# Kernel tuning notes

Measured on AMD Instinct MI355X. Metric: run time of the kernel, lower is better.

Reference implementation:

```python
import jax, jax.numpy as jnp
import numpy as np

N, F_IN, UNITS, HEADS = 8192, 256, 64, 4
NEG_BIG = -1e10


def setup_inputs() -> dict:
    key = jax.random.key(0)
    k1, k2, k3, k4, k5 = jax.random.split(key, 5)
    X = jax.random.normal(k1, (N, F_IN), dtype=jnp.float32)
    # sparse-ish binary adjacency with self-loops (float mask, as used by the module)
    A = (jax.random.uniform(k2, (N, N)) < 0.004).astype(jnp.float32)
    A = jnp.maximum(A, jnp.eye(N, dtype=jnp.float32))
    W = jax.random.normal(k3, (HEADS, F_IN, UNITS), dtype=jnp.float32) * (1.0 / np.sqrt(F_IN))
    attn_self = jax.random.normal(k4, (HEADS, UNITS), dtype=jnp.float32) * (1.0 / np.sqrt(UNITS))
    attn_neigh = jax.random.normal(k5, (HEADS, UNITS), dtype=jnp.float32) * (1.0 / np.sqrt(UNITS))
    return {"X": X, "A": A, "W": W, "attn_self": attn_self, "attn_neigh": attn_neigh}


def reference(X, A, W, attn_self, attn_neigh):
    # per-head linear projection: [H, N, U]
    feats = jnp.einsum('nf,hfu->hnu', X, W)
    a_self = jnp.einsum('hnu,hu->hn', feats, attn_self)    # [H, N]
    a_neigh = jnp.einsum('hnu,hu->hn', feats, attn_neigh)  # [H, N]
    # additive GAT scores: e_ij = a_self_i + a_neigh_j -> [H, N, N]
    scores = a_self[:, :, None] + a_neigh[:, None, :]
    scores = jax.nn.leaky_relu(scores, negative_slope=0.2)
    scores = scores + NEG_BIG * (1.0 - A)  # additive mask on non-edges
    attn = jax.nn.softmax(scores, axis=-1)
    # dropout is identity at training=False (module default)
    out = jnp.einsum('hnm,hmu->hnu', attn, feats)  # [H, N, U]
    # 'concat' reduction: head-major concat along feature dim -> [N, H*U]
    out = jnp.transpose(out, (1, 0, 2)).reshape(N, HEADS * UNITS)
    return jax.nn.elu(out)
```

## Files before the change

### kernel.cpp

```cpp
#include <hip/hip_runtime.h>
#include <hip/hip_bf16.h>

#define NN    8192
#define FIN   256
#define UNITS 64
#define HEADS 4
#define CTOT  256
#define CAP   256

__device__ __forceinline__ float bf2f(unsigned short u) {
    union { unsigned int i; float f; } v;
    v.i = ((unsigned int)u) << 16;
    return v.f;
}

__global__ void k_detect(const unsigned int* __restrict__ A, int* __restrict__ flag) {
    *flag = ((A[0] & 0xFFFFu) == 0x3F80u) ? 1 : 0;
}

__global__ __launch_bounds__(256) void k_proj(const void* __restrict__ Xv,
                                              const void* __restrict__ Wv,
                                              const int* __restrict__ flag,
                                              float* __restrict__ feats) {
    __shared__ float Xt[32 * 68];
    __shared__ float Wl[32 * 68];
    const int isbf = *flag;
    const int tid = threadIdx.x;
    const int r0  = blockIdx.x * 64;
    const int h   = blockIdx.y;

    const int r  = (tid & 15) * 4;
    const int cl = (tid >> 4) * 4;

    const int srow = tid >> 2;
    const int skq  = (tid & 3) * 8;
    const int wk   = tid >> 3;
    const int wu   = (tid & 7) * 8;

    float acc[4][4];
    #pragma unroll
    for (int a = 0; a < 4; ++a)
        #pragma unroll
        for (int b = 0; b < 4; ++b) acc[a][b] = 0.f;

    for (int k0 = 0; k0 < FIN; k0 += 32) {
        __syncthreads();
        if (isbf) {
            const unsigned short* X = (const unsigned short*)Xv;
            const unsigned short* W = (const unsigned short*)Wv;
            const uint4 xv = *reinterpret_cast<const uint4*>(
                X + (size_t)(r0 + srow) * FIN + k0 + skq);
            const unsigned int xs[4] = {xv.x, xv.y, xv.z, xv.w};
            #pragma unroll
            for (int m = 0; m < 4; ++m) {
                Xt[(skq + 2 * m    ) * 68 + srow] = bf2f((unsigned short)(xs[m] & 0xffffu));
                Xt[(skq + 2 * m + 1) * 68 + srow] = bf2f((unsigned short)(xs[m] >> 16));
            }
            const uint4 wv = *reinterpret_cast<const uint4*>(
                W + (size_t)h * (FIN * UNITS) + (size_t)(k0 + wk) * UNITS + wu);
            const unsigned int ws4[4] = {wv.x, wv.y, wv.z, wv.w};
            #pragma unroll
            for (int m = 0; m < 4; ++m) {
                Wl[wk * 68 + wu + 2 * m    ] = bf2f((unsigned short)(ws4[m] & 0xffffu));
                Wl[wk * 68 + wu + 2 * m + 1] = bf2f((unsigned short)(ws4[m] >> 16));
            }
        } else {
            const float* X = (const float*)Xv;
            const float* W = (const float*)Wv;
            const float4* xp = reinterpret_cast<const float4*>(
                X + (size_t)(r0 + srow) * FIN + k0 + skq);
            const float4 x0 = xp[0], x1 = xp[1];
            const float xs[8] = {x0.x, x0.y, x0.z, x0.w, x1.x, x1.y, x1.z, x1.w};
            #pragma unroll
            for (int m = 0; m < 8; ++m) Xt[(skq + m) * 68 + srow] = xs[m];
            const float4* wp = reinterpret_cast<const float4*>(
                W + (size_t)h * (FIN * UNITS) + (size_t)(k0 + wk) * UNITS + wu);
            const float4 w0 = wp[0], w1 = wp[1];
            const float ws8[8] = {w0.x, w0.y, w0.z, w0.w, w1.x, w1.y, w1.z, w1.w};
            #pragma unroll
            for (int m = 0; m < 8; ++m) Wl[wk * 68 + wu + m] = ws8[m];
        }
        __syncthreads();
        #pragma unroll 8
        for (int k = 0; k < 32; ++k) {
            const float4 a4 = *reinterpret_cast<const float4*>(&Xt[k * 68 + r]);
            const float4 b4 = *reinterpret_cast<const float4*>(&Wl[k * 68 + cl]);
            const float av[4] = {a4.x, a4.y, a4.z, a4.w};
            const float bv[4] = {b4.x, b4.y, b4.z, b4.w};
            #pragma unroll
            for (int ri = 0; ri < 4; ++ri)
                #pragma unroll
                for (int ci = 0; ci < 4; ++ci)
                    acc[ri][ci] += av[ri] * bv[ci];
        }
    }
    #pragma unroll
    for (int ri = 0; ri < 4; ++ri) {
        float4 o = make_float4(acc[ri][0], acc[ri][1], acc[ri][2], acc[ri][3]);
        *reinterpret_cast<float4*>(&feats[(size_t)(r0 + r + ri) * CTOT + h * UNITS + cl]) = o;
    }
}

__global__ __launch_bounds__(256) void k_attn_vec(const float* __restrict__ feats,
                                                  const void* __restrict__ attsv,
                                                  const void* __restrict__ attnv,
                                                  const int* __restrict__ flag,
                                                  float* __restrict__ s_self,
                                                  float* __restrict__ s_neigh) {
    const int isbf = *flag;
    const int tid  = threadIdx.x;
    const int w    = tid >> 6;
    const int lane = tid & 63;
    float as, an;
    if (isbf) {
        as = bf2f(((const unsigned short*)attsv)[w * UNITS + lane]);
        an = bf2f(((const unsigned short*)attnv)[w * UNITS + lane]);
    } else {
        as = ((const float*)attsv)[w * UNITS + lane];
        an = ((const float*)attnv)[w * UNITS + lane];
    }
    const int n0 = blockIdx.x * 8;
    for (int rr = 0; rr < 8; ++rr) {
        const int n = n0 + rr;
        const float v = feats[(size_t)n * CTOT + tid];
        float ss = v * as;
        float sn = v * an;
        #pragma unroll
        for (int off = 32; off > 0; off >>= 1) {
            ss += __shfl_xor(ss, off, 64);
            sn += __shfl_xor(sn, off, 64);
        }
        if (lane == 0) {
            s_self [w * NN + n] = ss;
            s_neigh[w * NN + n] = sn;
        }
    }
}

__global__ __launch_bounds__(256) void k_gat(const void* __restrict__ Av,
                                             const float* __restrict__ feats,
                                             const float* __restrict__ s_self,
                                             const float* __restrict__ s_neigh,
                                             const int* __restrict__ flag,
                                             void* __restrict__ outv) {
    __shared__ int   ej[CAP];
    __shared__ float sc[HEADS][CAP];
    __shared__ int   cnt;
    const int isbf = *flag;
    const int tid = threadIdx.x;
    const int i   = blockIdx.x;
    if (tid == 0) cnt = 0;
    __syncthreads();

    if (isbf) {
        const unsigned short* Arow = (const unsigned short*)Av + (size_t)i * NN;
        #pragma unroll
        for (int it = 0; it < 4; ++it) {
            const int j0 = it * 2048 + tid * 8;
            const uint4 v = *reinterpret_cast<const uint4*>(Arow + j0);
            const unsigned int vs[4] = {v.x, v.y, v.z, v.w};
            #pragma unroll
            for (int m = 0; m < 4; ++m) {
                if (vs[m] & 0xffffu) {
                    const int p = atomicAdd(&cnt, 1);
                    if (p < CAP) ej[p] = j0 + 2 * m;
                }
                if (vs[m] >> 16) {
                    const int p = atomicAdd(&cnt, 1);
                    if (p < CAP) ej[p] = j0 + 2 * m + 1;
                }
            }
        }
    } else {
        const float* Arow = (const float*)Av + (size_t)i * NN;
        #pragma unroll
        for (int it = 0; it < 4; ++it) {
            const int j0 = it * 2048 + tid * 8;
            const uint4 v0 = *reinterpret_cast<const uint4*>(Arow + j0);
            const uint4 v1 = *reinterpret_cast<const uint4*>(Arow + j0 + 4);
            const unsigned int vs[8] = {v0.x, v0.y, v0.z, v0.w, v1.x, v1.y, v1.z, v1.w};
            #pragma unroll
            for (int m = 0; m < 8; ++m) {
                if (vs[m] != 0u) {
                    const int p = atomicAdd(&cnt, 1);
                    if (p < CAP) ej[p] = j0 + m;
                }
            }
        }
    }
    __syncthreads();
    const int ne = min(cnt, CAP);

    float si[HEADS];
    #pragma unroll
    for (int h = 0; h < HEADS; ++h) si[h] = s_self[h * NN + i];
    for (int jj = tid; jj < ne; jj += 256) {
        const int j = ej[jj];
        #pragma unroll
        for (int h = 0; h < HEADS; ++h) {
            const float e = si[h] + s_neigh[h * NN + j];
            sc[h][jj] = (e > 0.f) ? e : 0.2f * e;
        }
    }
    __syncthreads();

    const int w    = tid >> 6;
    const int lane = tid & 63;
    float m = -3.0e38f;
    for (int jj = lane; jj < ne; jj += 64) m = fmaxf(m, sc[w][jj]);
    #pragma unroll
    for (int off = 32; off > 0; off >>= 1) m = fmaxf(m, __shfl_xor(m, off, 64));
    float l = 0.f;
    for (int jj = lane; jj < ne; jj += 64) {
        const float p = __expf(sc[w][jj] - m);
        sc[w][jj] = p;
        l += p;
    }
    #pragma unroll
    for (int off = 32; off > 0; off >>= 1) l += __shfl_xor(l, off, 64);
    const float rl = (l > 0.f) ? (1.f / l) : 0.f;

    float o = 0.f;
    for (int jj = 0; jj < ne; ++jj) {
        const int j = ej[jj];
        o += sc[w][jj] * feats[(size_t)j * CTOT + tid];
    }
    o *= rl;
    const float r = (o > 0.f) ? o : (__expf(o) - 1.f);

    if (isbf) {
        ((__hip_bfloat16*)outv)[(size_t)i * CTOT + tid] = __float2bfloat16(r);
    } else {
        ((float*)outv)[(size_t)i * CTOT + tid] = r;
    }
}

extern "C" void kernel_launch(void* const* d_in, const int* in_sizes, int n_in,
                              void* d_out, int out_size, void* d_ws, size_t ws_size,
                              hipStream_t stream) {
    const void* X    = d_in[0];
    const void* A    = d_in[1];
    const void* W    = d_in[2];
    const void* atts = d_in[3];
    const void* attn = d_in[4];

    float* feats   = (float*)d_ws;
    float* s_self  = feats  + (size_t)NN * CTOT;
    float* s_neigh = s_self + (size_t)HEADS * NN;
    int*   flag    = (int*)(s_neigh + (size_t)HEADS * NN);

    k_detect<<<1, 1, 0, stream>>>((const unsigned int*)A, flag);
    k_proj<<<dim3(NN / 64, HEADS), 256, 0, stream>>>(X, W, flag, feats);
    k_attn_vec<<<NN / 8, 256, 0, stream>>>(feats, atts, attn, flag, s_self, s_neigh);
    k_gat<<<NN, 256, 0, stream>>>(A, feats, s_self, s_neigh, flag, d_out);
}
```

Baseline: 405.2 us.

## Fuse attention-vector dot products into projection and compact adjacency scan with bitmasks

Removes the bf16 detection kernel and the separate attention-vector kernel. The per-node self and neighbour scores are now computed in the projection epilogue via shared-memory atomics and stored node-major. In the GAT kernel, each thread builds a bitmask of its nonzero adjacency entries and reserves slots with one atomic per thread instead of one per edge. Score computation is merged into the max pass, and the aggregation loop is unrolled by four with independent accumulators. The change drops bf16 input support and the guard against a zero softmax denominator.

```diff
diff --git a/kernel.cpp b/kernel.cpp
--- a/kernel.cpp
+++ b/kernel.cpp
@@ -1,5 +1,4 @@
 #include <hip/hip_runtime.h>
-#include <hip/hip_bf16.h>
 
 #define NN    8192
 #define FIN   256
@@ -8,23 +7,17 @@
 #define CTOT  256
 #define CAP   256
 
-__device__ __forceinline__ float bf2f(unsigned short u) {
-    union { unsigned int i; float f; } v;
-    v.i = ((unsigned int)u) << 16;
-    return v.f;
-}
-
-__global__ void k_detect(const unsigned int* __restrict__ A, int* __restrict__ flag) {
-    *flag = ((A[0] & 0xFFFFu) == 0x3F80u) ? 1 : 0;
-}
-
-__global__ __launch_bounds__(256) void k_proj(const void* __restrict__ Xv,
-                                              const void* __restrict__ Wv,
-                                              const int* __restrict__ flag,
-                                              float* __restrict__ feats) {
+__global__ __launch_bounds__(256) void k_proj(const float* __restrict__ X,
+                                              const float* __restrict__ W,
+                                              const float* __restrict__ atts,
+                                              const float* __restrict__ attn,
+                                              float* __restrict__ feats,
+                                              float* __restrict__ s_self,
+                                              float* __restrict__ s_neigh) {
     __shared__ float Xt[32 * 68];
     __shared__ float Wl[32 * 68];
-    const int isbf = *flag;
+    __shared__ float reds[64];
+    __shared__ float redn[64];
     const int tid = threadIdx.x;
     const int r0  = blockIdx.x * 64;
     const int h   = blockIdx.y;
@@ -37,6 +30,8 @@
     const int wk   = tid >> 3;
     const int wu   = (tid & 7) * 8;
 
+    if (tid < 64) { reds[tid] = 0.f; redn[tid] = 0.f; }
+
     float acc[4][4];
     #pragma unroll
     for (int a = 0; a < 4; ++a)
@@ -45,34 +40,15 @@
 
     for (int k0 = 0; k0 < FIN; k0 += 32) {
         __syncthreads();
-        if (isbf) {
-            const unsigned short* X = (const unsigned short*)Xv;
-            const unsigned short* W = (const unsigned short*)Wv;
-            const uint4 xv = *reinterpret_cast<const uint4*>(
-                X + (size_t)(r0 + srow) * FIN + k0 + skq);
-            const unsigned int xs[4] = {xv.x, xv.y, xv.z, xv.w};
-            #pragma unroll
-            for (int m = 0; m < 4; ++m) {
-                Xt[(skq + 2 * m    ) * 68 + srow] = bf2f((unsigned short)(xs[m] & 0xffffu));
-                Xt[(skq + 2 * m + 1) * 68 + srow] = bf2f((unsigned short)(xs[m] >> 16));
-            }
-            const uint4 wv = *reinterpret_cast<const uint4*>(
-                W + (size_t)h * (FIN * UNITS) + (size_t)(k0 + wk) * UNITS + wu);
-            const unsigned int ws4[4] = {wv.x, wv.y, wv.z, wv.w};
-            #pragma unroll
-            for (int m = 0; m < 4; ++m) {
-                Wl[wk * 68 + wu + 2 * m    ] = bf2f((unsigned short)(ws4[m] & 0xffffu));
-                Wl[wk * 68 + wu + 2 * m + 1] = bf2f((unsigned short)(ws4[m] >> 16));
-            }
-        } else {
-            const float* X = (const float*)Xv;
-            const float* W = (const float*)Wv;
+        {
             const float4* xp = reinterpret_cast<const float4*>(
                 X + (size_t)(r0 + srow) * FIN + k0 + skq);
             const float4 x0 = xp[0], x1 = xp[1];
             const float xs[8] = {x0.x, x0.y, x0.z, x0.w, x1.x, x1.y, x1.z, x1.w};
             #pragma unroll
             for (int m = 0; m < 8; ++m) Xt[(skq + m) * 68 + srow] = xs[m];
+        }
+        {
             const float4* wp = reinterpret_cast<const float4*>(
                 W + (size_t)h * (FIN * UNITS) + (size_t)(k0 + wk) * UNITS + wu);
             const float4 w0 = wp[0], w1 = wp[1];
@@ -94,120 +70,79 @@
                     acc[ri][ci] += av[ri] * bv[ci];
         }
     }
+
+    float as4[4], an4[4];
+    #pragma unroll
+    for (int ci = 0; ci < 4; ++ci) {
+        as4[ci] = atts[h * UNITS + cl + ci];
+        an4[ci] = attn[h * UNITS + cl + ci];
+    }
     #pragma unroll
     for (int ri = 0; ri < 4; ++ri) {
         float4 o = make_float4(acc[ri][0], acc[ri][1], acc[ri][2], acc[ri][3]);
         *reinterpret_cast<float4*>(&feats[(size_t)(r0 + r + ri) * CTOT + h * UNITS + cl]) = o;
+        const float ps = acc[ri][0] * as4[0] + acc[ri][1] * as4[1]
+                       + acc[ri][2] * as4[2] + acc[ri][3] * as4[3];
+        const float pn = acc[ri][0] * an4[0] + acc[ri][1] * an4[1]
+                       + acc[ri][2] * an4[2] + acc[ri][3] * an4[3];
+        atomicAdd(&reds[r + ri], ps);
+        atomicAdd(&redn[r + ri], pn);
+    }
+    __syncthreads();
+    if (tid < 64) {
+        s_self [((size_t)(r0 + tid) << 2) + h] = reds[tid];
+        s_neigh[((size_t)(r0 + tid) << 2) + h] = redn[tid];
     }
 }
 
-__global__ __launch_bounds__(256) void k_attn_vec(const float* __restrict__ feats,
-                                                  const void* __restrict__ attsv,
-                                                  const void* __restrict__ attnv,
-                                                  const int* __restrict__ flag,
-                                                  float* __restrict__ s_self,
-                                                  float* __restrict__ s_neigh) {
-    const int isbf = *flag;
-    const int tid  = threadIdx.x;
-    const int w    = tid >> 6;
-    const int lane = tid & 63;
-    float as, an;
-    if (isbf) {
-        as = bf2f(((const unsigned short*)attsv)[w * UNITS + lane]);
-        an = bf2f(((const unsigned short*)attnv)[w * UNITS + lane]);
-    } else {
-        as = ((const float*)attsv)[w * UNITS + lane];
-        an = ((const float*)attnv)[w * UNITS + lane];
-    }
-    const int n0 = blockIdx.x * 8;
-    for (int rr = 0; rr < 8; ++rr) {
-        const int n = n0 + rr;
-        const float v = feats[(size_t)n * CTOT + tid];
-        float ss = v * as;
-        float sn = v * an;
-        #pragma unroll
-        for (int off = 32; off > 0; off >>= 1) {
-            ss += __shfl_xor(ss, off, 64);
-            sn += __shfl_xor(sn, off, 64);
-        }
-        if (lane == 0) {
-            s_self [w * NN + n] = ss;
-            s_neigh[w * NN + n] = sn;
-        }
-    }
-}
-
-__global__ __launch_bounds__(256) void k_gat(const void* __restrict__ Av,
+__global__ __launch_bounds__(256) void k_gat(const float* __restrict__ A,
                                              const float* __restrict__ feats,
                                              const float* __restrict__ s_self,
                                              const float* __restrict__ s_neigh,
-                                             const int* __restrict__ flag,
-                                             void* __restrict__ outv) {
+                                             float* __restrict__ out) {
     __shared__ int   ej[CAP];
     __shared__ float sc[HEADS][CAP];
     __shared__ int   cnt;
-    const int isbf = *flag;
     const int tid = threadIdx.x;
     const int i   = blockIdx.x;
     if (tid == 0) cnt = 0;
     __syncthreads();
 
-    if (isbf) {
-        const unsigned short* Arow = (const unsigned short*)Av + (size_t)i * NN;
+    {
+        const float4* Arow4 = reinterpret_cast<const float4*>(A + (size_t)i * NN);
+        unsigned mask = 0;
         #pragma unroll
-        for (int it = 0; it < 4; ++it) {
-            const int j0 = it * 2048 + tid * 8;
-            const uint4 v = *reinterpret_cast<const uint4*>(Arow + j0);
-            const unsigned int vs[4] = {v.x, v.y, v.z, v.w};
-            #pragma unroll
-            for (int m = 0; m < 4; ++m) {
-                if (vs[m] & 0xffffu) {
-                    const int p = atomicAdd(&cnt, 1);
-                    if (p < CAP) ej[p] = j0 + 2 * m;
-                }
-                if (vs[m] >> 16) {
-                    const int p = atomicAdd(&cnt, 1);
-                    if (p < CAP) ej[p] = j0 + 2 * m + 1;
-                }
-            }
+        for (int q = 0; q < 8; ++q) {
+            const float4 v = Arow4[q * 256 + tid];
+            mask |= (v.x != 0.f ? 1u : 0u) << (4 * q);
+            mask |= (v.y != 0.f ? 1u : 0u) << (4 * q + 1);
+            mask |= (v.z != 0.f ? 1u : 0u) << (4 * q + 2);
+            mask |= (v.w != 0.f ? 1u : 0u) << (4 * q + 3);
         }
-    } else {
-        const float* Arow = (const float*)Av + (size_t)i * NN;
-        #pragma unroll
-        for (int it = 0; it < 4; ++it) {
-            const int j0 = it * 2048 + tid * 8;
-            const uint4 v0 = *reinterpret_cast<const uint4*>(Arow + j0);
-            const uint4 v1 = *reinterpret_cast<const uint4*>(Arow + j0 + 4);
-            const unsigned int vs[8] = {v0.x, v0.y, v0.z, v0.w, v1.x, v1.y, v1.z, v1.w};
-            #pragma unroll
-            for (int m = 0; m < 8; ++m) {
-                if (vs[m] != 0u) {
-                    const int p = atomicAdd(&cnt, 1);
-                    if (p < CAP) ej[p] = j0 + m;
-                }
-            }
+        const int c = __popc(mask);
+        int base = 0;
+        if (c) base = atomicAdd(&cnt, c);
+        while (mask) {
+            const int b = __ffs(mask) - 1;
+            mask &= mask - 1;
+            if (base < CAP) ej[base] = (b >> 2) * 1024 + tid * 4 + (b & 3);
+            ++base;
         }
     }
     __syncthreads();
     const int ne = min(cnt, CAP);
 
-    float si[HEADS];
-    #pragma unroll
-    for (int h = 0; h < HEADS; ++h) si[h] = s_self[h * NN + i];
-    for (int jj = tid; jj < ne; jj += 256) {
-        const int j = ej[jj];
-        #pragma unroll
-        for (int h = 0; h < HEADS; ++h) {
-            const float e = si[h] + s_neigh[h * NN + j];
-            sc[h][jj] = (e > 0.f) ? e : 0.2f * e;
-        }
-    }
-    __syncthreads();
-
     const int w    = tid >> 6;
     const int lane = tid & 63;
+    const float si = s_self[((size_t)i << 2) + w];
     float m = -3.0e38f;
-    for (int jj = lane; jj < ne; jj += 64) m = fmaxf(m, sc[w][jj]);
+    for (int jj = lane; jj < ne; jj += 64) {
+        const int j = ej[jj];
+        float e = si + s_neigh[((size_t)j << 2) + w];
+        e = (e > 0.f) ? e : 0.2f * e;
+        sc[w][jj] = e;
+        m = fmaxf(m, e);
+    }
     #pragma unroll
     for (int off = 32; off > 0; off >>= 1) m = fmaxf(m, __shfl_xor(m, off, 64));
     float l = 0.f;
@@ -218,39 +153,40 @@
     }
     #pragma unroll
     for (int off = 32; off > 0; off >>= 1) l += __shfl_xor(l, off, 64);
-    const float rl = (l > 0.f) ? (1.f / l) : 0.f;
+    const float rl = 1.f / l;
 
-    float o = 0.f;
-    for (int jj = 0; jj < ne; ++jj) {
-        const int j = ej[jj];
-        o += sc[w][jj] * feats[(size_t)j * CTOT + tid];
+    const float* fb = feats + tid;
+    float o0 = 0.f, o1 = 0.f, o2 = 0.f, o3 = 0.f;
+    int jj = 0;
+    for (; jj + 4 <= ne; jj += 4) {
+        const int ja = ej[jj], jb = ej[jj + 1], jc = ej[jj + 2], jd = ej[jj + 3];
+        const float pa = sc[w][jj],     pb = sc[w][jj + 1];
+        const float pc = sc[w][jj + 2], pd = sc[w][jj + 3];
+        o0 += pa * fb[(size_t)ja * CTOT];
+        o1 += pb * fb[(size_t)jb * CTOT];
+        o2 += pc * fb[(size_t)jc * CTOT];
+        o3 += pd * fb[(size_t)jd * CTOT];
     }
-    o *= rl;
-    const float r = (o > 0.f) ? o : (__expf(o) - 1.f);
-
-    if (isbf) {
-        ((__hip_bfloat16*)outv)[(size_t)i * CTOT + tid] = __float2bfloat16(r);
-    } else {
-        ((float*)outv)[(size_t)i * CTOT + tid] = r;
-    }
+    for (; jj < ne; ++jj) o0 += sc[w][jj] * fb[(size_t)ej[jj] * CTOT];
+    const float o = ((o0 + o1) + (o2 + o3)) * rl;
+    const float rr = (o > 0.f) ? o : (__expf(o) - 1.f);
+    out[(size_t)i * CTOT + tid] = rr;
 }
 
 extern "C" void kernel_launch(void* const* d_in, const int* in_sizes, int n_in,
                               void* d_out, int out_size, void* d_ws, size_t ws_size,
                               hipStream_t stream) {
-    const void* X    = d_in[0];
-    const void* A    = d_in[1];
-    const void* W    = d_in[2];
-    const void* atts = d_in[3];
-    const void* attn = d_in[4];
+    const float* X    = (const float*)d_in[0];
+    const float* A    = (const float*)d_in[1];
+    const float* W    = (const float*)d_in[2];
+    const float* atts = (const float*)d_in[3];
+    const float* attn = (const float*)d_in[4];
 
     float* feats   = (float*)d_ws;
     float* s_self  = feats  + (size_t)NN * CTOT;
-    float* s_neigh = s_self + (size_t)HEADS * NN;
-    int*   flag    = (int*)(s_neigh + (size_t)HEADS * NN);
+    float* s_neigh = s_self + (size_t)NN * HEADS;
 
-    k_detect<<<1, 1, 0, stream>>>((const unsigned int*)A, flag);
-    k_proj<<<dim3(NN / 64, HEADS), 256, 0, stream>>>(X, W, flag, feats);
-    k_attn_vec<<<NN / 8, 256, 0, stream>>>(feats, atts, attn, flag, s_self, s_neigh);
-    k_gat<<<NN, 256, 0, stream>>>(A, feats, s_self, s_neigh, flag, d_out);
+    k_proj<<<dim3(NN / 64, HEADS), 256, 0, stream>>>(X, W, atts, attn,
+                                                     feats, s_self, s_neigh);
+    k_gat<<<NN, 256, 0, stream>>>(A, feats, s_self, s_neigh, (float*)d_out);
 }
```

Measured after the change: 397.1 us. -2.0%, faster.
